# Optimization experiments

Hardware: AMD Instinct MI355X
Metric: run time of the kernel (lower is better)

Reference implementation:

```python
import jax, jax.numpy as jnp
import numpy as np


def setup_inputs() -> dict:
    key = jax.random.key(0)
    kq, kk, kv = jax.random.split(key, 3)
    B, S, D = 4, 4096, 64
    q = jax.random.normal(kq, (B, S, D), dtype=jnp.float32)
    k = jax.random.normal(kk, (B, S, D), dtype=jnp.float32)
    v = jax.random.normal(kv, (B, S, D), dtype=jnp.float32)
    return {"q": q, "k": k, "v": v}


def reference(q, k, v):
    # Faithful math of the original blocked loop:
    #   output_i += exp(Q_i @ K_j^T) @ V_j, summed over all column blocks j
    # which is exactly unnormalized exponential attention:
    #   out = exp(Q K^T) V  (no 1/sqrt(d) scaling, no softmax normalization,
    #   no max-subtraction -- matching the source module's math).
    scores = jnp.einsum("bqd,bkd->bqk", q, k)  # [B, Sq, Sk]
    return jnp.einsum("bqk,bkd->bqd", jnp.exp(scores), v)  # [B, Sq, D]
```

## Files before the change

kernel.cpp:

```cpp
#include <hip/hip_runtime.h>


typedef short    s16x4 __attribute__((ext_vector_type(4)));
typedef short    s16x8 __attribute__((ext_vector_type(8)));
typedef _Float16 h16x8 __attribute__((ext_vector_type(8)));
typedef float    fx4   __attribute__((ext_vector_type(4)));

constexpr int S = 4096, D = 64, BQ = 64, BN = 128;
constexpr int TILES  = S / BN;
constexpr int CHUNKS = 16;
constexpr int BATCH_HALVES = S * D;
constexpr int TILE_STRIDE  = TILES * CHUNKS * 64 * 8;

__device__ __forceinline__ unsigned short f2bf(float x) {
    unsigned u = __float_as_uint(x);
    u = (u + 0x7FFFu + ((u >> 16) & 1u)) >> 16;
    return (unsigned short)u;
}
__device__ __forceinline__ float bf2f(unsigned short h) {
    return __uint_as_float(((unsigned)h) << 16);
}
__device__ __forceinline__ unsigned short f2h(float x) {
    union { _Float16 h; unsigned short s; } u;
    u.h = (_Float16)x;
    return u.s;
}

__global__ __launch_bounds__(256) void prep_kernel(
    const float* __restrict__ k, const float* __restrict__ v,
    unsigned short* __restrict__ kf, unsigned short* __restrict__ vfr)
{
    const int id = blockIdx.x * 256 + threadIdx.x;
    const int KTOT = 4 * TILES * CHUNKS * 64;
    if (id < KTOT) {
        const int l = id & 63, c = (id >> 6) & 15, t = (id >> 10) & 31, b = id >> 15;
        const int row = t * BN + (c >> 1) * 16 + (l & 15);
        const int dd  = (c & 1) * 32 + (l >> 4) * 8;
        const float* src = k + ((size_t)b * S + row) * D + dd;
        float4 f0 = *(const float4*)src;
        float4 f1 = *(const float4*)(src + 4);
        s16x8 o = { (short)f2h(f0.x), (short)f2h(f0.y), (short)f2h(f0.z), (short)f2h(f0.w),
                    (short)f2h(f1.x), (short)f2h(f1.y), (short)f2h(f1.z), (short)f2h(f1.w) };
        *(s16x8*)(kf + (size_t)id * 8) = o;
    } else {
        const int vid = id - KTOT;
        const int l = vid & 63, c2 = (vid >> 6) & 15, t = (vid >> 10) & 31, b = vid >> 15;
        const int kk0 = t * BN + (c2 >> 2) * 32 + (l >> 4) * 8;
        const int dc  = (c2 & 3) * 16 + (l & 15);
        const float* src = v + ((size_t)b * S + kk0) * D + dc;
        s16x8 o;
        #pragma unroll
        for (int j = 0; j < 8; ++j) o[j] = (short)f2bf(src[(size_t)j * D]);
        *(s16x8*)(vfr + (size_t)vid * 8) = o;
    }
}

__global__ __launch_bounds__(512) void attn_main(
    const float* __restrict__ q, const unsigned short* __restrict__ kf,
    const unsigned short* __restrict__ vfr, float* __restrict__ out)
{
    __shared__ unsigned short Kbuf[2][CHUNKS * 64 * 8];
    __shared__ unsigned short Vbuf[2][CHUNKS * 64 * 8];
    __shared__ unsigned short Pm[BQ][136];

    const int tid  = threadIdx.x;
    const int lane = tid & 63;
    const int w    = tid >> 6;
    const int quad = lane >> 4;
    const int tq   = lane & 15;
    const int ksup = w & 3, msup = w >> 2;
    const int h = w & 1, dq = (w >> 1) & 1, mq = w >> 2;

    const int b  = blockIdx.y;
    const int q0 = blockIdx.x * BQ;
    const unsigned short* kfb = kf  + (size_t)b * TILE_STRIDE;
    const unsigned short* vfb = vfr + (size_t)b * TILE_STRIDE;
    float* ob = out + (size_t)b * S * D;

    h16x8 qf[2][2];
    #pragma unroll
    for (int msub = 0; msub < 2; ++msub)
        #pragma unroll
        for (int ks = 0; ks < 2; ++ks) {
            const float* src = q + ((size_t)b * S + q0 + msup * 32 + msub * 16 + tq) * D
                             + ks * 32 + quad * 8;
            float4 f0 = *(const float4*)src;
            float4 f1 = *(const float4*)(src + 4);
            h16x8 qv = { (_Float16)f0.x, (_Float16)f0.y, (_Float16)f0.z, (_Float16)f0.w,
                         (_Float16)f1.x, (_Float16)f1.y, (_Float16)f1.z, (_Float16)f1.w };
            qf[msub][ks] = qv;
        }

    fx4 oacc[2][2] = {};

    auto issue_tile = [&](int tt, int bi) {
        #pragma unroll
        for (int ii = 0; ii < 2; ++ii) {
            const int c = w + ii * 8;
            const size_t goff = ((size_t)(tt * CHUNKS + c) * 64 + lane) * 8;
            __builtin_amdgcn_global_load_lds(
                (const __attribute__((address_space(1))) unsigned int*)(kfb + goff),
                (__attribute__((address_space(3))) unsigned int*)&Kbuf[bi][(c * 64 + lane) * 8],
                16, 0, 0);
            __builtin_amdgcn_global_load_lds(
                (const __attribute__((address_space(1))) unsigned int*)(vfb + goff),
                (__attribute__((address_space(3))) unsigned int*)&Vbuf[bi][(c * 64 + lane) * 8],
                16, 0, 0);
        }
    };

    issue_tile(0, 0);

    for (int t = 0; t < TILES; ++t) {
        const int cur = t & 1;
        __syncthreads();
        issue_tile((t + 1) & (TILES - 1), cur ^ 1);

        fx4 sacc[2][2] = {};
        #pragma unroll
        for (int ks = 0; ks < 2; ++ks)
            #pragma unroll
            for (int kks = 0; kks < 2; ++kks) {
                const int c = (ksup * 2 + kks) * 2 + ks;
                h16x8 a = *(const h16x8*)&Kbuf[cur][(c * 64 + lane) * 8];
                #pragma unroll
                for (int msub = 0; msub < 2; ++msub)
                    sacc[kks][msub] = __builtin_amdgcn_mfma_f32_16x16x32_f16(
                        a, qf[msub][ks], sacc[kks][msub], 0, 0, 0);
            }

        #pragma unroll
        for (int kks = 0; kks < 2; ++kks)
            #pragma unroll
            for (int msub = 0; msub < 2; ++msub) {
                s16x4 pp = { (short)f2bf(__expf(sacc[kks][msub][0])),
                             (short)f2bf(__expf(sacc[kks][msub][1])),
                             (short)f2bf(__expf(sacc[kks][msub][2])),
                             (short)f2bf(__expf(sacc[kks][msub][3])) };
                *(s16x4*)&Pm[msup * 32 + msub * 16 + tq]
                            [ksup * 32 + kks * 16 + (quad << 2)] = pp;
            }

        __asm__ volatile("" ::: "memory");
        __builtin_amdgcn_s_waitcnt(0xC07F);
        __builtin_amdgcn_s_barrier();
        __asm__ volatile("" ::: "memory");

        #pragma unroll
        for (int i = 0; i < 2; ++i) {
            const int ks2 = h * 2 + i;
            s16x8 bfr[2];
            #pragma unroll
            for (int dsub = 0; dsub < 2; ++dsub)
                bfr[dsub] = *(const s16x8*)&Vbuf[cur]
                                [((ks2 * 4 + dq * 2 + dsub) * 64 + lane) * 8];
            #pragma unroll
            for (int msub = 0; msub < 2; ++msub) {
                s16x8 afr = *(const s16x8*)&Pm[mq * 32 + msub * 16 + tq]
                                              [ks2 * 32 + (quad << 3)];
                #pragma unroll
                for (int dsub = 0; dsub < 2; ++dsub)
                    oacc[msub][dsub] = __builtin_amdgcn_mfma_f32_16x16x32_bf16(
                        afr, bfr[dsub], oacc[msub][dsub], 0, 0, 0);
            }
        }
    }

    __syncthreads();
    fx4* red = (fx4*)&Kbuf[0][0];
    const int p = w >> 1;
    if (h == 1) {
        #pragma unroll
        for (int msub = 0; msub < 2; ++msub)
            #pragma unroll
            for (int dsub = 0; dsub < 2; ++dsub)
                red[p * 256 + lane * 4 + msub * 2 + dsub] = oacc[msub][dsub];
    }
    __syncthreads();
    if (h == 0) {
        #pragma unroll
        for (int msub = 0; msub < 2; ++msub)
            #pragma unroll
            for (int dsub = 0; dsub < 2; ++dsub) {
                fx4 val = oacc[msub][dsub] + red[p * 256 + lane * 4 + msub * 2 + dsub];
                #pragma unroll
                for (int r = 0; r < 4; ++r)
                    ob[(size_t)(q0 + mq * 32 + msub * 16 + quad * 4 + r) * D
                       + dq * 32 + dsub * 16 + tq] = val[r];
            }
    }
}

__global__ __launch_bounds__(1024) void attn_fallback(
    const float* __restrict__ q, const float* __restrict__ k,
    const float* __restrict__ v, float* __restrict__ out)
{
    __shared__ unsigned short Kh[64][72];
    __shared__ unsigned short Kl[64][72];
    __shared__ unsigned short Vt[64][68];
    __shared__ unsigned short Pf[64][72];

    const int tid = threadIdx.x, lane = tid & 63, wave = tid >> 6;
    const int quad = lane >> 4, tq = lane & 15;
    const int kkb = wave & 3, mba = wave >> 2;
    const int b = blockIdx.y, q0 = blockIdx.x * 64;
    const float* qb = q + (size_t)b * S * D;
    const float* kb = k + (size_t)b * S * D;
    const float* vb = v + (size_t)b * S * D;
    float* ob = out + (size_t)b * S * D;

    s16x8 qh[2], ql[2];
    {
        const float* qrow = qb + (size_t)(q0 + mba * 16 + tq) * D;
        #pragma unroll
        for (int ks = 0; ks < 2; ++ks) {
            const float* src = qrow + ks * 32 + quad * 8;
            float4 f0 = *(const float4*)src;
            float4 f1 = *(const float4*)(src + 4);
            float f[8] = {f0.x, f0.y, f0.z, f0.w, f1.x, f1.y, f1.z, f1.w};
            #pragma unroll
            for (int j = 0; j < 8; ++j) {
                unsigned short hh = f2bf(f[j]);
                qh[ks][j] = (short)hh;
                ql[ks][j] = (short)f2bf(f[j] - bf2f(hh));
            }
        }
    }
    fx4 oacc = {0.f, 0.f, 0.f, 0.f};
    const int krow = tid >> 4, kc4 = (tid & 15) << 2;
    const int vd = tid & 63, vk = (tid >> 6) << 2;

    for (int t = 0; t < S / 64; ++t) {
        __syncthreads();
        const float* kt = kb + (size_t)(t * 64 + krow) * D;
        const float* vt = vb + (size_t)(t * 64 + vk) * D;
        {
            float4 kv = *(const float4*)(kt + kc4);
            unsigned short h0 = f2bf(kv.x), h1 = f2bf(kv.y), h2 = f2bf(kv.z), h3 = f2bf(kv.w);
            s16x4 a = {(short)h0, (short)h1, (short)h2, (short)h3};
            s16x4 l4 = {(short)f2bf(kv.x - bf2f(h0)), (short)f2bf(kv.y - bf2f(h1)),
                        (short)f2bf(kv.z - bf2f(h2)), (short)f2bf(kv.w - bf2f(h3))};
            *(s16x4*)&Kh[krow][kc4] = a;
            *(s16x4*)&Kl[krow][kc4] = l4;
            const float* vs = vt + vd;
            s16x4 vv = {(short)f2bf(vs[0]), (short)f2bf(vs[D]),
                        (short)f2bf(vs[2 * D]), (short)f2bf(vs[3 * D])};
            *(s16x4*)&Vt[vd][vk] = vv;
        }
        __syncthreads();
        fx4 sacc = {0.f, 0.f, 0.f, 0.f};
        #pragma unroll
        for (int ks = 0; ks < 2; ++ks) {
            s16x8 kah = *(const s16x8*)&Kh[kkb * 16 + tq][ks * 32 + quad * 8];
            s16x8 kal = *(const s16x8*)&Kl[kkb * 16 + tq][ks * 32 + quad * 8];
            sacc = __builtin_amdgcn_mfma_f32_16x16x32_bf16(kah, qh[ks], sacc, 0, 0, 0);
            sacc = __builtin_amdgcn_mfma_f32_16x16x32_bf16(kah, ql[ks], sacc, 0, 0, 0);
            sacc = __builtin_amdgcn_mfma_f32_16x16x32_bf16(kal, qh[ks], sacc, 0, 0, 0);
        }
        s16x4 pp = {(short)f2bf(__expf(sacc[0])), (short)f2bf(__expf(sacc[1])),
                    (short)f2bf(__expf(sacc[2])), (short)f2bf(__expf(sacc[3]))};
        *(s16x4*)&Pf[mba * 16 + tq][kkb * 16 + (quad << 2)] = pp;
        __syncthreads();
        #pragma unroll
        for (int ks = 0; ks < 2; ++ks) {
            s16x8 pa = *(const s16x8*)&Pf[mba * 16 + tq][ks * 32 + quad * 8];
            const unsigned short* vr = &Vt[kkb * 16 + tq][ks * 32 + quad * 8];
            s16x4 va = *(const s16x4*)vr;
            s16x4 vb2 = *(const s16x4*)(vr + 4);
            s16x8 vfull = __builtin_shufflevector(va, vb2, 0, 1, 2, 3, 4, 5, 6, 7);
            oacc = __builtin_amdgcn_mfma_f32_16x16x32_bf16(pa, vfull, oacc, 0, 0, 0);
        }
    }
    #pragma unroll
    for (int r = 0; r < 4; ++r)
        ob[(size_t)(q0 + mba * 16 + quad * 4 + r) * D + kkb * 16 + tq] = oacc[r];
}

extern "C" void kernel_launch(void* const* d_in, const int* in_sizes, int n_in,
                              void* d_out, int out_size, void* d_ws, size_t ws_size,
                              hipStream_t stream) {
    const float* q = (const float*)d_in[0];
    const float* k = (const float*)d_in[1];
    const float* v = (const float*)d_in[2];
    float* out = (float*)d_out;
    const int nbatch = in_sizes[0] / (S * D);

    const size_t need = (size_t)nbatch * S * D * 2 * 2;
    if (nbatch == 4 && ws_size >= need && d_ws != nullptr) {
        unsigned short* kf  = (unsigned short*)d_ws;
        unsigned short* vfr = kf + (size_t)nbatch * S * D;
        const int total = 2 * nbatch * TILES * CHUNKS * 64;
        prep_kernel<<<total / 256, 256, 0, stream>>>(k, v, kf, vfr);
        dim3 grid(S / BQ, nbatch);
        attn_main<<<grid, 512, 0, stream>>>(q, kf, vfr, out);
    } else {
        dim3 grid(S / 64, nbatch);
        attn_fallback<<<grid, 1024, 0, stream>>>(q, k, v, out);
    }
}
```

Measured before the change: 106.3 us.

## Switch attention to 32x32 MFMA with register-resident P and triple-buffered tiles

Rewrites the main kernel to use 32x32x16 MFMA tiles. The exp(QK^T) probabilities stay in registers, exchanged between lane halves with a cross-lane shuffle, so the shared-memory P round-trip and its barrier are gone. K/V tiles are triple-buffered with a two-tile prefetch depth and a partial vmcnt wait, so only one barrier is needed per iteration. The prep kernel is rewritten to stage K/V through shared memory for coalesced reads and a fragment layout matching the new MFMA shape. The costs are a larger LDS footprint, which may reduce occupancy, and a four-way cross-wave reduction at the end.

```diff
diff --git a/kernel.cpp b/kernel.cpp
--- a/kernel.cpp
+++ b/kernel.cpp
@@ -5,12 +5,12 @@
 typedef short    s16x8 __attribute__((ext_vector_type(8)));
 typedef _Float16 h16x8 __attribute__((ext_vector_type(8)));
 typedef float    fx4   __attribute__((ext_vector_type(4)));
+typedef float    fx16  __attribute__((ext_vector_type(16)));
 
 constexpr int S = 4096, D = 64, BQ = 64, BN = 128;
-constexpr int TILES  = S / BN;
-constexpr int CHUNKS = 16;
-constexpr int BATCH_HALVES = S * D;
-constexpr int TILE_STRIDE  = TILES * CHUNKS * 64 * 8;
+constexpr int TILES = S / BN;
+constexpr int TILE_SHORTS  = 16 * 512;
+constexpr int BATCH_SHORTS = TILES * TILE_SHORTS;
 
 __device__ __forceinline__ unsigned short f2bf(float x) {
     unsigned u = __float_as_uint(x);
@@ -26,167 +26,166 @@
     return u.s;
 }
 
-__global__ __launch_bounds__(256) void prep_kernel(
+__global__ __launch_bounds__(256) void prep2(
     const float* __restrict__ k, const float* __restrict__ v,
-    unsigned short* __restrict__ kf, unsigned short* __restrict__ vfr)
+    unsigned short* __restrict__ kf, unsigned short* __restrict__ vf)
 {
-    const int id = blockIdx.x * 256 + threadIdx.x;
-    const int KTOT = 4 * TILES * CHUNKS * 64;
-    if (id < KTOT) {
-        const int l = id & 63, c = (id >> 6) & 15, t = (id >> 10) & 31, b = id >> 15;
-        const int row = t * BN + (c >> 1) * 16 + (l & 15);
-        const int dd  = (c & 1) * 32 + (l >> 4) * 8;
-        const float* src = k + ((size_t)b * S + row) * D + dd;
-        float4 f0 = *(const float4*)src;
-        float4 f1 = *(const float4*)(src + 4);
-        s16x8 o = { (short)f2h(f0.x), (short)f2h(f0.y), (short)f2h(f0.z), (short)f2h(f0.w),
-                    (short)f2h(f1.x), (short)f2h(f1.y), (short)f2h(f1.z), (short)f2h(f1.w) };
-        *(s16x8*)(kf + (size_t)id * 8) = o;
-    } else {
-        const int vid = id - KTOT;
-        const int l = vid & 63, c2 = (vid >> 6) & 15, t = (vid >> 10) & 31, b = vid >> 15;
-        const int kk0 = t * BN + (c2 >> 2) * 32 + (l >> 4) * 8;
-        const int dc  = (c2 & 3) * 16 + (l & 15);
-        const float* src = v + ((size_t)b * S + kk0) * D + dc;
+    __shared__ unsigned short tile[128 * 72];
+    const int tid   = threadIdx.x;
+    const int which = blockIdx.x & 1;
+    const int t     = (blockIdx.x >> 1) & 31;
+    const int b     = blockIdx.x >> 6;
+    const float* src = (which ? v : k) + ((size_t)b * S + t * BN) * D;
+
+    #pragma unroll
+    for (int i = 0; i < 8; ++i) {
+        int f   = i * 256 + tid;
+        int row = f >> 4;
+        int c4  = (f & 15) << 2;
+        float4 x = *(const float4*)(src + row * D + c4);
+        s16x4 o;
+        if (which) o = (s16x4){(short)f2bf(x.x), (short)f2bf(x.y),
+                               (short)f2bf(x.z), (short)f2bf(x.w)};
+        else       o = (s16x4){(short)f2h(x.x), (short)f2h(x.y),
+                               (short)f2h(x.z), (short)f2h(x.w)};
+        *(s16x4*)&tile[row * 72 + c4] = o;
+    }
+    __syncthreads();
+
+    const int lane = tid & 63;
+    unsigned short* dst = (which ? vf : kf) + (size_t)b * BATCH_SHORTS + t * TILE_SHORTS;
+    #pragma unroll
+    for (int i = 0; i < 4; ++i) {
+        int c = (tid >> 6) * 4 + i;
         s16x8 o;
-        #pragma unroll
-        for (int j = 0; j < 8; ++j) o[j] = (short)f2bf(src[(size_t)j * D]);
-        *(s16x8*)(vfr + (size_t)vid * 8) = o;
-    }
-}
-
-__global__ __launch_bounds__(512) void attn_main(
+        if (which == 0) {
+            int row = (c >> 2) * 32 + (lane & 31);
+            int dc  = (c & 3) * 16 + (lane >> 5) * 8;
+            o = *(const s16x8*)&tile[row * 72 + dc];
+        } else {
+            int r0 = (c >> 1) * 16 + (lane >> 5) * 8;
+            int dc = (c & 1) * 32 + (lane & 31);
+            #pragma unroll
+            for (int j = 0; j < 8; ++j) o[j] = (short)tile[(r0 + j) * 72 + dc];
+        }
+        *(s16x8*)(dst + c * 512 + lane * 8) = o;
+    }
+}
+
+__global__ __launch_bounds__(512) void attn_main2(
     const float* __restrict__ q, const unsigned short* __restrict__ kf,
-    const unsigned short* __restrict__ vfr, float* __restrict__ out)
+    const unsigned short* __restrict__ vf, float* __restrict__ out)
 {
-    __shared__ unsigned short Kbuf[2][CHUNKS * 64 * 8];
-    __shared__ unsigned short Vbuf[2][CHUNKS * 64 * 8];
-    __shared__ unsigned short Pm[BQ][136];
-
-    const int tid  = threadIdx.x;
-    const int lane = tid & 63;
-    const int w    = tid >> 6;
-    const int quad = lane >> 4;
-    const int tq   = lane & 15;
-    const int ksup = w & 3, msup = w >> 2;
-    const int h = w & 1, dq = (w >> 1) & 1, mq = w >> 2;
-
-    const int b  = blockIdx.y;
-    const int q0 = blockIdx.x * BQ;
-    const unsigned short* kfb = kf  + (size_t)b * TILE_STRIDE;
-    const unsigned short* vfb = vfr + (size_t)b * TILE_STRIDE;
-    float* ob = out + (size_t)b * S * D;
-
-    h16x8 qf[2][2];
-    #pragma unroll
-    for (int msub = 0; msub < 2; ++msub)
-        #pragma unroll
-        for (int ks = 0; ks < 2; ++ks) {
-            const float* src = q + ((size_t)b * S + q0 + msup * 32 + msub * 16 + tq) * D
-                             + ks * 32 + quad * 8;
-            float4 f0 = *(const float4*)src;
-            float4 f1 = *(const float4*)(src + 4);
-            h16x8 qv = { (_Float16)f0.x, (_Float16)f0.y, (_Float16)f0.z, (_Float16)f0.w,
-                         (_Float16)f1.x, (_Float16)f1.y, (_Float16)f1.z, (_Float16)f1.w };
-            qf[msub][ks] = qv;
-        }
-
-    fx4 oacc[2][2] = {};
-
-    auto issue_tile = [&](int tt, int bi) {
-        #pragma unroll
-        for (int ii = 0; ii < 2; ++ii) {
-            const int c = w + ii * 8;
-            const size_t goff = ((size_t)(tt * CHUNKS + c) * 64 + lane) * 8;
+    __shared__ unsigned short smem[3 * 2 * TILE_SHORTS];
+
+    const int tid = threadIdx.x, lane = tid & 63, w = tid >> 6;
+    const int h = lane >> 5, m5 = lane & 31;
+    const int mt = w & 1, kkq = w >> 1;
+    const int b = blockIdx.y, q0 = blockIdx.x * BQ;
+
+    const unsigned short* kfb = kf + (size_t)b * BATCH_SHORTS;
+    const unsigned short* vfb = vf + (size_t)b * BATCH_SHORTS;
+
+    h16x8 qf[4];
+    {
+        const float* qrow = q + ((size_t)b * S + q0 + mt * 32 + m5) * D + h * 8;
+        #pragma unroll
+        for (int ks = 0; ks < 4; ++ks) {
+            float4 a = *(const float4*)(qrow + ks * 16);
+            float4 c = *(const float4*)(qrow + ks * 16 + 4);
+            qf[ks] = (h16x8){(_Float16)a.x, (_Float16)a.y, (_Float16)a.z, (_Float16)a.w,
+                             (_Float16)c.x, (_Float16)c.y, (_Float16)c.z, (_Float16)c.w};
+        }
+    }
+
+    fx16 oacc[2] = {};
+
+    auto issue = [&](int t, int bi) {
+        unsigned short* base = &smem[bi * 2 * TILE_SHORTS];
+        #pragma unroll
+        for (int ii = 0; ii < 4; ++ii) {
+            int c = (ii & 1) * 8 + w;
+            const unsigned short* g = (ii < 2 ? kfb : vfb)
+                + (size_t)t * TILE_SHORTS + c * 512 + lane * 8;
+            unsigned short* l = base + (ii < 2 ? 0 : TILE_SHORTS) + c * 512 + lane * 8;
             __builtin_amdgcn_global_load_lds(
-                (const __attribute__((address_space(1))) unsigned int*)(kfb + goff),
-                (__attribute__((address_space(3))) unsigned int*)&Kbuf[bi][(c * 64 + lane) * 8],
-                16, 0, 0);
-            __builtin_amdgcn_global_load_lds(
-                (const __attribute__((address_space(1))) unsigned int*)(vfb + goff),
-                (__attribute__((address_space(3))) unsigned int*)&Vbuf[bi][(c * 64 + lane) * 8],
-                16, 0, 0);
+                (const __attribute__((address_space(1))) unsigned int*)g,
+                (__attribute__((address_space(3))) unsigned int*)l, 16, 0, 0);
         }
     };
 
-    issue_tile(0, 0);
+    issue(0, 0);
+    issue(1, 1);
 
     for (int t = 0; t < TILES; ++t) {
-        const int cur = t & 1;
-        __syncthreads();
-        issue_tile((t + 1) & (TILES - 1), cur ^ 1);
-
-        fx4 sacc[2][2] = {};
-        #pragma unroll
-        for (int ks = 0; ks < 2; ++ks)
-            #pragma unroll
-            for (int kks = 0; kks < 2; ++kks) {
-                const int c = (ksup * 2 + kks) * 2 + ks;
-                h16x8 a = *(const h16x8*)&Kbuf[cur][(c * 64 + lane) * 8];
-                #pragma unroll
-                for (int msub = 0; msub < 2; ++msub)
-                    sacc[kks][msub] = __builtin_amdgcn_mfma_f32_16x16x32_f16(
-                        a, qf[msub][ks], sacc[kks][msub], 0, 0, 0);
-            }
-
-        #pragma unroll
-        for (int kks = 0; kks < 2; ++kks)
-            #pragma unroll
-            for (int msub = 0; msub < 2; ++msub) {
-                s16x4 pp = { (short)f2bf(__expf(sacc[kks][msub][0])),
-                             (short)f2bf(__expf(sacc[kks][msub][1])),
-                             (short)f2bf(__expf(sacc[kks][msub][2])),
-                             (short)f2bf(__expf(sacc[kks][msub][3])) };
-                *(s16x4*)&Pm[msup * 32 + msub * 16 + tq]
-                            [ksup * 32 + kks * 16 + (quad << 2)] = pp;
-            }
-
+        const int bi = t % 3;
         __asm__ volatile("" ::: "memory");
-        __builtin_amdgcn_s_waitcnt(0xC07F);
+        __builtin_amdgcn_s_waitcnt(0x0F74);
         __builtin_amdgcn_s_barrier();
         __asm__ volatile("" ::: "memory");
-
-        #pragma unroll
-        for (int i = 0; i < 2; ++i) {
-            const int ks2 = h * 2 + i;
-            s16x8 bfr[2];
-            #pragma unroll
-            for (int dsub = 0; dsub < 2; ++dsub)
-                bfr[dsub] = *(const s16x8*)&Vbuf[cur]
-                                [((ks2 * 4 + dq * 2 + dsub) * 64 + lane) * 8];
-            #pragma unroll
-            for (int msub = 0; msub < 2; ++msub) {
-                s16x8 afr = *(const s16x8*)&Pm[mq * 32 + msub * 16 + tq]
-                                              [ks2 * 32 + (quad << 3)];
+        issue((t + 2) & (TILES - 1), (t + 2) % 3);
+
+        const unsigned short* kb = &smem[bi * 2 * TILE_SHORTS];
+        const unsigned short* vb = kb + TILE_SHORTS;
+
+        fx16 sa = {};
+        #pragma unroll
+        for (int ks = 0; ks < 4; ++ks) {
+            h16x8 a = *(const h16x8*)(kb + (kkq * 4 + ks) * 512 + lane * 8);
+            sa = __builtin_amdgcn_mfma_f32_32x32x16_f16(a, qf[ks], sa, 0, 0, 0);
+        }
+
+        unsigned p01[8], sw[8];
+        #pragma unroll
+        for (int r = 0; r < 8; ++r) {
+            unsigned lo = f2bf(__expf(sa[2 * r]));
+            unsigned hi = f2bf(__expf(sa[2 * r + 1]));
+            p01[r] = lo | (hi << 16);
+        }
+        #pragma unroll
+        for (int r = 0; r < 8; ++r) sw[r] = (unsigned)__shfl_xor((int)p01[r], 32, 64);
+
+        union { unsigned u[4]; s16x8 v; } A1u, A2u;
+        A1u.u[0] = h ? sw[2]  : p01[0];  A1u.u[1] = h ? sw[3]  : p01[1];
+        A1u.u[2] = h ? p01[2] : sw[0];   A1u.u[3] = h ? p01[3] : sw[1];
+        A2u.u[0] = h ? sw[6]  : p01[4];  A2u.u[1] = h ? sw[7]  : p01[5];
+        A2u.u[2] = h ? p01[6] : sw[4];   A2u.u[3] = h ? p01[7] : sw[5];
+
+        #pragma unroll
+        for (int u = 0; u < 2; ++u) {
+            s16x8 Au = u ? A2u.v : A1u.v;
+            int ss = kkq * 2 + u;
+            #pragma unroll
+            for (int dt = 0; dt < 2; ++dt) {
+                s16x8 vv = *(const s16x8*)(vb + (ss * 2 + dt) * 512 + lane * 8);
+                oacc[dt] = __builtin_amdgcn_mfma_f32_32x32x16_bf16(Au, vv, oacc[dt], 0, 0, 0);
+            }
+        }
+    }
+
+    __syncthreads();
+    float* scratch = (float*)smem;
+    if (kkq > 0) {
+        float* dst = scratch + (size_t)(mt * 3 + (kkq - 1)) * 2048;
+        #pragma unroll
+        for (int dt = 0; dt < 2; ++dt)
+            #pragma unroll
+            for (int r = 0; r < 16; ++r)
+                dst[(dt * 16 + r) * 64 + lane] = oacc[dt][r];
+    }
+    __syncthreads();
+    if (kkq == 0) {
+        float* ob = out + (size_t)b * S * D;
+        #pragma unroll
+        for (int dt = 0; dt < 2; ++dt)
+            #pragma unroll
+            for (int r = 0; r < 16; ++r) {
+                float val = oacc[dt][r];
                 #pragma unroll
-                for (int dsub = 0; dsub < 2; ++dsub)
-                    oacc[msub][dsub] = __builtin_amdgcn_mfma_f32_16x16x32_bf16(
-                        afr, bfr[dsub], oacc[msub][dsub], 0, 0, 0);
-            }
-        }
-    }
-
-    __syncthreads();
-    fx4* red = (fx4*)&Kbuf[0][0];
-    const int p = w >> 1;
-    if (h == 1) {
-        #pragma unroll
-        for (int msub = 0; msub < 2; ++msub)
-            #pragma unroll
-            for (int dsub = 0; dsub < 2; ++dsub)
-                red[p * 256 + lane * 4 + msub * 2 + dsub] = oacc[msub][dsub];
-    }
-    __syncthreads();
-    if (h == 0) {
-        #pragma unroll
-        for (int msub = 0; msub < 2; ++msub)
-            #pragma unroll
-            for (int dsub = 0; dsub < 2; ++dsub) {
-                fx4 val = oacc[msub][dsub] + red[p * 256 + lane * 4 + msub * 2 + dsub];
-                #pragma unroll
-                for (int r = 0; r < 4; ++r)
-                    ob[(size_t)(q0 + mq * 32 + msub * 16 + quad * 4 + r) * D
-                       + dq * 32 + dsub * 16 + tq] = val[r];
+                for (int p = 0; p < 3; ++p)
+                    val += scratch[(size_t)(mt * 3 + p) * 2048 + (dt * 16 + r) * 64 + lane];
+                int row = q0 + mt * 32 + (r & 3) + 8 * (r >> 2) + 4 * h;
+                ob[(size_t)row * D + dt * 32 + m5] = val;
             }
     }
 }
@@ -287,12 +286,11 @@
 
     const size_t need = (size_t)nbatch * S * D * 2 * 2;
     if (nbatch == 4 && ws_size >= need && d_ws != nullptr) {
-        unsigned short* kf  = (unsigned short*)d_ws;
-        unsigned short* vfr = kf + (size_t)nbatch * S * D;
-        const int total = 2 * nbatch * TILES * CHUNKS * 64;
-        prep_kernel<<<total / 256, 256, 0, stream>>>(k, v, kf, vfr);
+        unsigned short* kf = (unsigned short*)d_ws;
+        unsigned short* vf = kf + (size_t)nbatch * S * D;
+        prep2<<<nbatch * TILES * 2, 256, 0, stream>>>(k, v, kf, vf);
         dim3 grid(S / BQ, nbatch);
-        attn_main<<<grid, 512, 0, stream>>>(q, kf, vfr, out);
+        attn_main2<<<grid, 512, 0, stream>>>(q, kf, vf, out);
     } else {
         dim3 grid(S / 64, nbatch);
         attn_fallback<<<grid, 1024, 0, stream>>>(q, k, v, out);
```

After: 98.01 us. 7.8% less time.
